# Performance work log

Hardware: AMD Instinct MI355X
Metric: run time of the kernel (lower is better)

Reference implementation:

```python
import jax, jax.numpy as jnp
import numpy as np

B, S, D = 4, 1024, 1024
H, HD = 16, 64
MAXPOS = 1024  # max_position_embeddings


def setup_inputs() -> dict:
    key = jax.random.key(0)
    ks = jax.random.split(key, 10)
    sc = 0.02
    return {
        "hidden_states": jax.random.normal(ks[0], (B, S, D), dtype=jnp.float32),
        "attention_mask": jnp.zeros((B, 1, 1, S), dtype=jnp.float32),
        "across_attention_prior": jax.random.uniform(ks[1], (B, H, S, S), dtype=jnp.float32),
        "head_mask": jnp.ones((1, H, 1, 1), dtype=jnp.float32),
        "Wq": jax.random.normal(ks[2], (D, D), dtype=jnp.float32) * sc,
        "bq": jnp.zeros((D,), dtype=jnp.float32),
        "Wk": jax.random.normal(ks[3], (D, D), dtype=jnp.float32) * sc,
        "bk": jnp.zeros((D,), dtype=jnp.float32),
        "Wv": jax.random.normal(ks[4], (D, D), dtype=jnp.float32) * sc,
        "bv": jnp.zeros((D,), dtype=jnp.float32),
        "dist_emb": jax.random.normal(ks[5], (2 * MAXPOS - 1, HD), dtype=jnp.float32) * sc,
    }


def _heads(x):
    # [B,S,D] -> [B,H,S,HD]
    return x.reshape(B, S, H, HD).transpose(0, 2, 1, 3)


def reference(hidden_states, attention_mask, across_attention_prior, head_mask,
              Wq, bq, Wk, bk, Wv, bv, dist_emb):
    q = _heads(hidden_states @ Wq + bq)  # [B,H,S,HD]
    k = _heads(hidden_states @ Wk + bk)
    v = _heads(hidden_states @ Wv + bv)

    scores = jnp.einsum("bhld,bhrd->bhlr", q, k)

    # relative_key_query positional bias
    pos = jnp.arange(S)
    distance = pos[:, None] - pos[None, :]  # [S,S]
    pe = dist_emb[distance + MAXPOS - 1]  # [S,S,HD] (l, r, d)
    scores = scores + jnp.einsum("bhld,lrd->bhlr", q, pe)
    scores = scores + jnp.einsum("bhrd,lrd->bhlr", k, pe)

    scores = scores / jnp.sqrt(jnp.float32(HD))
    scores = scores + attention_mask  # additive mask, broadcast [B,1,1,S]

    probs = jax.nn.softmax(scores, axis=-1)
    probs = probs * across_attention_prior  # post-softmax multiplicative prior
    probs = probs * head_mask  # dropout prob = 0 (eval)

    ctx = jnp.einsum("bhlr,bhrd->bhld", probs, v)
    ctx = ctx.transpose(0, 2, 1, 3).reshape(B, S, D)
    return ctx
```

## Files before the change

kernel.cpp:

```cpp
#include <hip/hip_runtime.h>


typedef unsigned short u16;
typedef unsigned int   u32;
typedef __attribute__((ext_vector_type(8))) short bfx8;
typedef __attribute__((ext_vector_type(4))) float f32x4;

#define MFMA_BF16(a, b, c) __builtin_amdgcn_mfma_f32_16x16x32_bf16(a, b, c, 0, 0, 0)

__device__ __forceinline__ u16 f2bf(float f) {
    union { float f; u32 u; } c; c.f = f;
    u32 u = c.u;
    return (u16)((u + 0x7FFFu + ((u >> 16) & 1u)) >> 16);
}
__device__ __forceinline__ float bf2f(u16 v) {
    union { u32 u; float f; } c; c.u = ((u32)v) << 16;
    return c.f;
}
__device__ __forceinline__ float load_f(const void* p, long i, bool bf) {
    return bf ? bf2f(((const u16*)p)[i]) : ((const float*)p)[i];
}
__device__ __forceinline__ u16 load_bf(const void* p, long i, bool bf) {
    return bf ? ((const u16*)p)[i] : f2bf(((const float*)p)[i]);
}

__device__ __forceinline__ void gload16(const u16* g, u16* l) {
    __builtin_amdgcn_global_load_lds(
        (__attribute__((address_space(1))) void*)g,
        (__attribute__((address_space(3))) void*)l, 16, 0, 0);
}

__device__ __forceinline__ void wg_barrier() {
    asm volatile("s_waitcnt lgkmcnt(0)" ::: "memory");
    __builtin_amdgcn_s_barrier();
    asm volatile("" ::: "memory");
}

__global__ void k_detect(const u32* hid, int* flags) {
    __shared__ int cnt;
    if (threadIdx.x == 0) cnt = 0;
    __syncthreads();
    int c = 0;
    for (int i = threadIdx.x; i < 1024; i += 256) {
        u32 w = hid[i];
        u32 e = (w >> 7) & 0xFFu;
        if (e >= 100u && e <= 140u) c++;
    }
    atomicAdd(&cnt, c);
    __syncthreads();
    if (threadIdx.x == 0) flags[0] = (cnt > 512) ? 1 : 0;
}

__global__ void k_prep(const void* hidden, const void* dist, const void* mask,
                       const void* hm, const void* bq, const void* bk,
                       const void* bv, const int* flags, u16* hid_bf,
                       u16* dist_bf, float* mask_f, float* hm_f, float* bias_f) {
    const bool bf = flags[0] != 0;
    const long NH = 4L * 1024 * 1024, ND = 2047L * 64, NM = 4096, NB = 3072, NHM = 16;
    const long TOT = NH + ND + NM + NB + NHM;
    for (long i = (long)blockIdx.x * 256 + threadIdx.x; i < TOT;
         i += (long)gridDim.x * 256) {
        if (i < NH) hid_bf[i] = load_bf(hidden, i, bf);
        else if (i < NH + ND) dist_bf[i - NH] = load_bf(dist, i - NH, bf);
        else if (i < NH + ND + NM) mask_f[i - NH - ND] = load_f(mask, i - NH - ND, bf);
        else if (i < NH + ND + NM + NB) {
            long j = i - NH - ND - NM;
            const void* src = (j < 1024) ? bq : ((j < 2048) ? bk : bv);
            bias_f[j] = load_f(src, j & 1023, bf);
        } else {
            long j = i - NH - ND - NM - NB;
            hm_f[j] = load_f(hm, j, bf);
        }
    }
}

__global__ void k_transpose(const void* Wq, const void* Wk, const void* Wv,
                            const int* flags, u16* wt) {
    const bool bf = flags[0] != 0;
    __shared__ float t[32][33];
    const int z = blockIdx.z;
    const void* W = (z == 0) ? Wq : ((z == 1) ? Wk : Wv);
    int x = blockIdx.x * 32 + threadIdx.x;
    for (int i = 0; i < 4; i++) {
        int y = blockIdx.y * 32 + threadIdx.y + i * 8;
        t[threadIdx.y + i * 8][threadIdx.x] = load_f(W, (long)y * 1024 + x, bf);
    }
    __syncthreads();
    int x2 = blockIdx.y * 32 + threadIdx.x;
    u16* out = wt + (long)z * 1024 * 1024;
    for (int i = 0; i < 4; i++) {
        int y2 = blockIdx.x * 32 + threadIdx.y + i * 8;
        out[(long)y2 * 1024 + x2] = f2bf(t[threadIdx.x][threadIdx.y + i * 8]);
    }
}

__global__ __launch_bounds__(256, 2)
void k_qkv_gemm(const u16* A, const u16* Bt, const float* bias,
                u16* qb, u16* kb, u16* vb) {
    __shared__ u16 sA[128 * 32];
    __shared__ u16 sB[128 * 32];
    const int tid = threadIdx.x;
    const int w = tid >> 6, lane = tid & 63;
    const int quad = lane >> 4, nl = lane & 15;
    const int wr = w >> 1, wc = w & 1;
    const int n0 = blockIdx.x * 128, m0 = blockIdx.y * 128;

    f32x4 acc[4][4];
#pragma unroll
    for (int a = 0; a < 4; a++)
#pragma unroll
        for (int b = 0; b < 4; b++) acc[a][b] = (f32x4){0.f, 0.f, 0.f, 0.f};

    for (int kt = 0; kt < 32; kt++) {
        const int k0 = kt * 32;
        __syncthreads();
#pragma unroll
        for (int j = 0; j < 2; j++) {
            int row = 32 * w + 16 * j + (lane >> 2);
            int seg = lane & 3;
            gload16(A + (long)(m0 + row) * 1024 + k0 + seg * 8, sA + 1024 * w + 512 * j);
            gload16(Bt + (long)(n0 + row) * 1024 + k0 + seg * 8, sB + 1024 * w + 512 * j);
        }
        __syncthreads();

        bfx8 af[4], bfr[4];
#pragma unroll
        for (int f = 0; f < 4; f++) {
            af[f]  = *(const bfx8*)(sA + (64 * wr + 16 * f + nl) * 32 + quad * 8);
            bfr[f] = *(const bfx8*)(sB + (64 * wc + 16 * f + nl) * 32 + quad * 8);
        }
#pragma unroll
        for (int fm = 0; fm < 4; fm++)
#pragma unroll
            for (int fn = 0; fn < 4; fn++)
                acc[fm][fn] = MFMA_BF16(af[fm], bfr[fn], acc[fm][fn]);
    }

#pragma unroll
    for (int fm = 0; fm < 4; fm++) {
#pragma unroll
        for (int fn = 0; fn < 4; fn++) {
            int n = n0 + 64 * wc + 16 * fn + nl;
            int which = n >> 10, hcol = n & 1023;
            int h = hcol >> 6, hd = hcol & 63;
            u16* op = (which == 0) ? qb : ((which == 1) ? kb : vb);
            float bias_v = bias[n];
#pragma unroll
            for (int reg = 0; reg < 4; reg++) {
                int m = m0 + 64 * wr + 16 * fm + 4 * quad + reg;
                int b = m >> 10, s = m & 1023;
                float v = acc[fm][fn][reg] + bias_v;
                op[((long)((b * 16 + h) * 1024 + s)) * 64 + hd] = f2bf(v);
            }
        }
    }
}

__global__ __launch_bounds__(256, 2)
void k_attn(const u16* qb, const u16* kb, const u16* vb, const u16* Eb,
            const float* maskf, const float* hmf, const void* prior,
            const int* flags, void* out) {
    constexpr int PT = 72;
    constexpr int PD = 132;
    __shared__ __align__(16) char smem[79872];
    u16* sQ  = (u16*)(smem);
    u16* sK  = (u16*)(smem + 9216);
    u16* sVT = (u16*)(smem + 18432);
    u16* sE  = (u16*)(smem + 27648);
    u16* sDq = (u16*)(smem + 46080);
    u16* sDk = (u16*)(smem + 62976);
    u16* sP  = (u16*)(smem + 46080);

    const int tid = threadIdx.x;
    const int w = tid >> 6, lane = tid & 63;
    const int quad = lane >> 4, nl = lane & 15;
    const int bh = blockIdx.x, b = bh >> 4, h = bh & 15;
    const int l0 = blockIdx.y * 64;
    const bool bf = flags[0] != 0;

    const u16* qbh = qb + (long)bh * 65536;
    const u16* kbh = kb + (long)bh * 65536;
    const u16* vbh = vb + (long)bh * 65536;

#pragma unroll
    for (int p = 0; p < 2; p++) {
        int seg = tid + p * 256;
        int row = seg >> 3, s8 = seg & 7;
        *(int4*)(sQ + row * PT + s8 * 8) = *(const int4*)(qbh + (l0 + row) * 64 + s8 * 8);
    }

    const int erow = tid >> 3, es8 = tid & 7;
    const int jb_base = l0 + 960;

    int4 nK0, nK1, nE0, nE1, nE2, nE3, nV0, nV1;
    {
        nK0 = *(const int4*)(kbh + (0 + erow) * 64 + es8 * 8);
        nK1 = *(const int4*)(kbh + (32 + erow) * 64 + es8 * 8);
        int j0 = jb_base + erow;       if (j0 > 2046) j0 = 2046;
        int j1 = jb_base + 32 + erow;  if (j1 > 2046) j1 = 2046;
        int j2 = jb_base + 64 + erow;  if (j2 > 2046) j2 = 2046;
        int j3 = jb_base + 96 + erow;  if (j3 > 2046) j3 = 2046;
        nE0 = *(const int4*)(Eb + (long)j0 * 64 + es8 * 8);
        nE1 = *(const int4*)(Eb + (long)j1 * 64 + es8 * 8);
        nE2 = *(const int4*)(Eb + (long)j2 * 64 + es8 * 8);
        nE3 = *(const int4*)(Eb + (long)j3 * 64 + es8 * 8);
        nV0 = *(const int4*)(vbh + (0 + lane) * 64 + w * 8);
        nV1 = *(const int4*)(vbh + (0 + lane) * 64 + w * 8 + 32);
    }

    f32x4 accv[4];
#pragma unroll
    for (int f = 0; f < 4; f++) accv[f] = (f32x4){0.f, 0.f, 0.f, 0.f};
    float zacc[4] = {0.f, 0.f, 0.f, 0.f};

    for (int it = 0; it < 16; it++) {
        const int r0 = it * 64;
        wg_barrier();

        *(int4*)(sK + erow * PT + es8 * 8)        = nK0;
        *(int4*)(sK + (32 + erow) * PT + es8 * 8) = nK1;
        *(int4*)(sE + erow * PT + es8 * 8)        = nE0;
        *(int4*)(sE + (32 + erow) * PT + es8 * 8) = nE1;
        *(int4*)(sE + (64 + erow) * PT + es8 * 8) = nE2;
        *(int4*)(sE + (96 + erow) * PT + es8 * 8) = nE3;
        {
            const u16* pv0 = (const u16*)&nV0;
            const u16* pv1 = (const u16*)&nV1;
#pragma unroll
            for (int j2 = 0; j2 < 8; j2++) {
                sVT[(w * 8 + j2) * PT + lane]      = pv0[j2];
                sVT[(w * 8 + 32 + j2) * PT + lane] = pv1[j2];
            }
        }

        float pr[4][4], mval[4];
#pragma unroll
        for (int fn = 0; fn < 4; fn++) {
            mval[fn] = maskf[b * 1024 + r0 + fn * 16 + nl];
#pragma unroll
            for (int reg = 0; reg < 4; reg++) {
                long pidx = ((long)(bh * 1024 + l0 + 16 * w + 4 * quad + reg)) * 1024
                            + r0 + fn * 16 + nl;
                pr[fn][reg] = bf ? bf2f(((const u16*)prior)[pidx])
                                 : ((const float*)prior)[pidx];
            }
        }

        if (it < 15) {
            const int r0n = r0 + 64;
            const int jbn = jb_base - r0n;
            nK0 = *(const int4*)(kbh + (r0n + erow) * 64 + es8 * 8);
            nK1 = *(const int4*)(kbh + (r0n + 32 + erow) * 64 + es8 * 8);
            int j0 = jbn + erow;       if (j0 > 2046) j0 = 2046;
            int j1 = jbn + 32 + erow;  if (j1 > 2046) j1 = 2046;
            int j2 = jbn + 64 + erow;  if (j2 > 2046) j2 = 2046;
            int j3 = jbn + 96 + erow;  if (j3 > 2046) j3 = 2046;
            nE0 = *(const int4*)(Eb + (long)j0 * 64 + es8 * 8);
            nE1 = *(const int4*)(Eb + (long)j1 * 64 + es8 * 8);
            nE2 = *(const int4*)(Eb + (long)j2 * 64 + es8 * 8);
            nE3 = *(const int4*)(Eb + (long)j3 * 64 + es8 * 8);
            nV0 = *(const int4*)(vbh + (r0n + lane) * 64 + w * 8);
            nV1 = *(const int4*)(vbh + (r0n + lane) * 64 + w * 8 + 32);
        }
        wg_barrier();

        bfx8 aq0 = *(const bfx8*)(sQ + (16 * w + nl) * PT + quad * 8);
        bfx8 aq1 = *(const bfx8*)(sQ + (16 * w + nl) * PT + quad * 8 + 32);
        bfx8 ak0 = *(const bfx8*)(sK + (16 * w + nl) * PT + quad * 8);
        bfx8 ak1 = *(const bfx8*)(sK + (16 * w + nl) * PT + quad * 8 + 32);

#pragma unroll
        for (int fc = 0; fc < 8; fc++) {
            bfx8 be0 = *(const bfx8*)(sE + (fc * 16 + nl) * PT + quad * 8);
            bfx8 be1 = *(const bfx8*)(sE + (fc * 16 + nl) * PT + quad * 8 + 32);
            f32x4 dq = (f32x4){0.f, 0.f, 0.f, 0.f};
            dq = MFMA_BF16(aq0, be0, dq);
            dq = MFMA_BF16(aq1, be1, dq);
            f32x4 dk = (f32x4){0.f, 0.f, 0.f, 0.f};
            dk = MFMA_BF16(ak0, be0, dk);
            dk = MFMA_BF16(ak1, be1, dk);
#pragma unroll
            for (int reg = 0; reg < 4; reg++) {
                int rr = 16 * w + 4 * quad + reg;
                sDq[rr * PD + fc * 16 + nl] = f2bf(dq[reg]);
                sDk[rr * PD + fc * 16 + nl] = f2bf(dk[reg]);
            }
        }
        f32x4 accs[4];
#pragma unroll
        for (int fn = 0; fn < 4; fn++) {
            bfx8 bk0 = *(const bfx8*)(sK + (fn * 16 + nl) * PT + quad * 8);
            bfx8 bk1 = *(const bfx8*)(sK + (fn * 16 + nl) * PT + quad * 8 + 32);
            f32x4 s = (f32x4){0.f, 0.f, 0.f, 0.f};
            s = MFMA_BF16(aq0, bk0, s);
            s = MFMA_BF16(aq1, bk1, s);
            accs[fn] = s;
        }
        wg_barrier();

        float pw[4][4];
#pragma unroll
        for (int fn = 0; fn < 4; fn++) {
#pragma unroll
            for (int reg = 0; reg < 4; reg++) {
                int li = 16 * w + 4 * quad + reg;
                int ri = 16 * fn + nl;
                int u = li - ri + 63;
                float s = (accs[fn][reg] + bf2f(sDq[li * PD + u])
                           + bf2f(sDk[ri * PD + u])) * 0.125f + mval[fn];
                float e = __expf(s);
                zacc[reg] += e;
                pw[fn][reg] = e * pr[fn][reg];
            }
        }
        wg_barrier();

#pragma unroll
        for (int fn = 0; fn < 4; fn++)
#pragma unroll
            for (int reg = 0; reg < 4; reg++)
                sP[(16 * w + 4 * quad + reg) * PT + fn * 16 + nl] = f2bf(pw[fn][reg]);

        bfx8 ap0 = *(const bfx8*)(sP + (16 * w + nl) * PT + quad * 8);
        bfx8 ap1 = *(const bfx8*)(sP + (16 * w + nl) * PT + quad * 8 + 32);
#pragma unroll
        for (int fd = 0; fd < 4; fd++) {
            bfx8 bv0 = *(const bfx8*)(sVT + (fd * 16 + nl) * PT + quad * 8);
            bfx8 bv1 = *(const bfx8*)(sVT + (fd * 16 + nl) * PT + quad * 8 + 32);
            accv[fd] = MFMA_BF16(ap0, bv0, accv[fd]);
            accv[fd] = MFMA_BF16(ap1, bv1, accv[fd]);
        }
    }

#pragma unroll
    for (int reg = 0; reg < 4; reg++) {
        float z = zacc[reg];
        z += __shfl_xor(z, 1);
        z += __shfl_xor(z, 2);
        z += __shfl_xor(z, 4);
        z += __shfl_xor(z, 8);
        zacc[reg] = z;
    }
    const float hm = hmf[h];
#pragma unroll
    for (int fd = 0; fd < 4; fd++) {
#pragma unroll
        for (int reg = 0; reg < 4; reg++) {
            int l = l0 + 16 * w + 4 * quad + reg;
            int d = fd * 16 + nl;
            float val = accv[fd][reg] * hm / zacc[reg];
            long oidx = ((long)(b * 1024 + l)) * 1024 + h * 64 + d;
            if (bf) ((u16*)out)[oidx] = f2bf(val);
            else    ((float*)out)[oidx] = val;
        }
    }
}

extern "C" void kernel_launch(void* const* d_in, const int* in_sizes, int n_in,
                              void* d_out, int out_size, void* d_ws, size_t ws_size,
                              hipStream_t stream) {
    char* ws = (char*)d_ws;
    int*   flags   = (int*)ws;
    u16*   hid_bf  = (u16*)(ws + 256);
    u16*   wt_bf   = (u16*)(ws + 8388864);
    u16*   dist_bf = (u16*)(ws + 14680320);
    float* mask_f  = (float*)(ws + 14942464);
    float* bias_f  = (float*)(ws + 14958848);
    float* hm_f    = (float*)(ws + 14971136);
    u16*   q_bf    = (u16*)(ws + 14971392);
    u16*   k_bf    = (u16*)(ws + 23360000);
    u16*   v_bf    = (u16*)(ws + 31748608);

    k_detect<<<1, 256, 0, stream>>>((const u32*)d_in[0], flags);
    k_prep<<<2048, 256, 0, stream>>>(d_in[0], d_in[10], d_in[1], d_in[3],
                                     d_in[5], d_in[7], d_in[9], flags,
                                     hid_bf, dist_bf, mask_f, hm_f, bias_f);
    k_transpose<<<dim3(32, 32, 3), dim3(32, 8), 0, stream>>>(
        d_in[4], d_in[6], d_in[8], flags, wt_bf);
    k_qkv_gemm<<<dim3(24, 32), 256, 0, stream>>>(hid_bf, wt_bf, bias_f,
                                                 q_bf, k_bf, v_bf);
    k_attn<<<dim3(64, 16), 256, 0, stream>>>(q_bf, k_bf, v_bf, dist_bf,
                                             mask_f, hm_f, d_in[2], flags, d_out);
}
```

Baseline: 522.9 us.

## Split attention key tiles across 8 waves and widen QKV GEMM K-tile with swizzle

The attention kernel now runs 512 threads per block. Each pair of waves splits the 64-key tile in half, and the partial P·V accumulators and softmax denominators are combined through shared memory at the end. Q fragments are hoisted out of the loop. The QKV GEMM moves to a 64-wide K tile with XOR-swizzled shared layout and a remapped block order, aiming to reduce bank conflicts and synchronisation count and to improve L2 locality. The risks are higher register pressure under the new launch bounds, the extra cross-wave reduction, and whether 79 KB of shared memory per block allows the intended occupancy.

```diff
diff --git a/kernel.cpp b/kernel.cpp
--- a/kernel.cpp
+++ b/kernel.cpp
@@ -97,13 +97,15 @@
 __global__ __launch_bounds__(256, 2)
 void k_qkv_gemm(const u16* A, const u16* Bt, const float* bias,
                 u16* qb, u16* kb, u16* vb) {
-    __shared__ u16 sA[128 * 32];
-    __shared__ u16 sB[128 * 32];
+    __shared__ u16 sA[128 * 64];
+    __shared__ u16 sB[128 * 64];
     const int tid = threadIdx.x;
     const int w = tid >> 6, lane = tid & 63;
     const int quad = lane >> 4, nl = lane & 15;
     const int wr = w >> 1, wc = w & 1;
-    const int n0 = blockIdx.x * 128, m0 = blockIdx.y * 128;
+    const int bid0 = blockIdx.y * 24 + blockIdx.x;
+    const int bid = (bid0 & 7) * 96 + (bid0 >> 3);
+    const int n0 = (bid % 24) * 128, m0 = (bid / 24) * 128;
 
     f32x4 acc[4][4];
 #pragma unroll
@@ -111,29 +113,39 @@
 #pragma unroll
         for (int b = 0; b < 4; b++) acc[a][b] = (f32x4){0.f, 0.f, 0.f, 0.f};
 
-    for (int kt = 0; kt < 32; kt++) {
-        const int k0 = kt * 32;
+    const int srow = 32 * w + (lane >> 3);
+    const int seg = lane & 7;
+
+    for (int kt = 0; kt < 16; kt++) {
+        const int k0 = kt * 64;
         __syncthreads();
 #pragma unroll
-        for (int j = 0; j < 2; j++) {
-            int row = 32 * w + 16 * j + (lane >> 2);
-            int seg = lane & 3;
-            gload16(A + (long)(m0 + row) * 1024 + k0 + seg * 8, sA + 1024 * w + 512 * j);
-            gload16(Bt + (long)(n0 + row) * 1024 + k0 + seg * 8, sB + 1024 * w + 512 * j);
+        for (int j = 0; j < 4; j++) {
+            int row = srow + 8 * j;
+            int ss = (seg ^ (row & 7)) * 8;
+            gload16(A + (long)(m0 + row) * 1024 + k0 + ss, sA + (32 * w + 8 * j) * 64);
+            gload16(Bt + (long)(n0 + row) * 1024 + k0 + ss, sB + (32 * w + 8 * j) * 64);
         }
         __syncthreads();
 
-        bfx8 af[4], bfr[4];
+        bfx8 af[4][2], bfr[4][2];
 #pragma unroll
         for (int f = 0; f < 4; f++) {
-            af[f]  = *(const bfx8*)(sA + (64 * wr + 16 * f + nl) * 32 + quad * 8);
-            bfr[f] = *(const bfx8*)(sB + (64 * wc + 16 * f + nl) * 32 + quad * 8);
+#pragma unroll
+            for (int hh = 0; hh < 2; hh++) {
+                int Ra = 64 * wr + 16 * f + nl;
+                int Rb = 64 * wc + 16 * f + nl;
+                af[f][hh]  = *(const bfx8*)(sA + Ra * 64 + (((4 * hh + quad) ^ (Ra & 7)) * 8));
+                bfr[f][hh] = *(const bfx8*)(sB + Rb * 64 + (((4 * hh + quad) ^ (Rb & 7)) * 8));
+            }
         }
 #pragma unroll
         for (int fm = 0; fm < 4; fm++)
 #pragma unroll
-            for (int fn = 0; fn < 4; fn++)
-                acc[fm][fn] = MFMA_BF16(af[fm], bfr[fn], acc[fm][fn]);
+            for (int fn = 0; fn < 4; fn++) {
+                acc[fm][fn] = MFMA_BF16(af[fm][0], bfr[fn][0], acc[fm][fn]);
+                acc[fm][fn] = MFMA_BF16(af[fm][1], bfr[fn][1], acc[fm][fn]);
+            }
     }
 
 #pragma unroll
@@ -156,12 +168,13 @@
     }
 }
 
-__global__ __launch_bounds__(256, 2)
+__global__ __launch_bounds__(512, 4)
 void k_attn(const u16* qb, const u16* kb, const u16* vb, const u16* Eb,
             const float* maskf, const float* hmf, const void* prior,
             const int* flags, void* out) {
     constexpr int PT = 72;
     constexpr int PD = 132;
+    constexpr int PX = 66;
     __shared__ __align__(16) char smem[79872];
     u16* sQ  = (u16*)(smem);
     u16* sK  = (u16*)(smem + 9216);
@@ -170,9 +183,12 @@
     u16* sDq = (u16*)(smem + 46080);
     u16* sDk = (u16*)(smem + 62976);
     u16* sP  = (u16*)(smem + 46080);
+    float* accx = (float*)(smem + 46080);
+    float* zs   = (float*)(smem + 9216);
 
     const int tid = threadIdx.x;
-    const int w = tid >> 6, lane = tid & 63;
+    const int W = tid >> 6, lane = tid & 63;
+    const int s = W >> 1, c = W & 1;
     const int quad = lane >> 4, nl = lane & 15;
     const int bh = blockIdx.x, b = bh >> 4, h = bh & 15;
     const int l0 = blockIdx.y * 64;
@@ -182,31 +198,27 @@
     const u16* kbh = kb + (long)bh * 65536;
     const u16* vbh = vb + (long)bh * 65536;
 
-#pragma unroll
-    for (int p = 0; p < 2; p++) {
-        int seg = tid + p * 256;
-        int row = seg >> 3, s8 = seg & 7;
+    {
+        int row = tid >> 3, s8 = tid & 7;
         *(int4*)(sQ + row * PT + s8 * 8) = *(const int4*)(qbh + (l0 + row) * 64 + s8 * 8);
     }
 
     const int erow = tid >> 3, es8 = tid & 7;
     const int jb_base = l0 + 960;
 
-    int4 nK0, nK1, nE0, nE1, nE2, nE3, nV0, nV1;
+    int4 nK0, nE0, nE1, nV0;
     {
-        nK0 = *(const int4*)(kbh + (0 + erow) * 64 + es8 * 8);
-        nK1 = *(const int4*)(kbh + (32 + erow) * 64 + es8 * 8);
+        nK0 = *(const int4*)(kbh + erow * 64 + es8 * 8);
         int j0 = jb_base + erow;       if (j0 > 2046) j0 = 2046;
-        int j1 = jb_base + 32 + erow;  if (j1 > 2046) j1 = 2046;
-        int j2 = jb_base + 64 + erow;  if (j2 > 2046) j2 = 2046;
-        int j3 = jb_base + 96 + erow;  if (j3 > 2046) j3 = 2046;
+        int j1 = jb_base + 64 + erow;  if (j1 > 2046) j1 = 2046;
         nE0 = *(const int4*)(Eb + (long)j0 * 64 + es8 * 8);
         nE1 = *(const int4*)(Eb + (long)j1 * 64 + es8 * 8);
-        nE2 = *(const int4*)(Eb + (long)j2 * 64 + es8 * 8);
-        nE3 = *(const int4*)(Eb + (long)j3 * 64 + es8 * 8);
-        nV0 = *(const int4*)(vbh + (0 + lane) * 64 + w * 8);
-        nV1 = *(const int4*)(vbh + (0 + lane) * 64 + w * 8 + 32);
-    }
+        nV0 = *(const int4*)(vbh + lane * 64 + W * 8);
+    }
+
+    wg_barrier();
+    const bfx8 aq0 = *(const bfx8*)(sQ + (16 * s + nl) * PT + quad * 8);
+    const bfx8 aq1 = *(const bfx8*)(sQ + (16 * s + nl) * PT + quad * 8 + 32);
 
     f32x4 accv[4];
 #pragma unroll
@@ -218,30 +230,24 @@
         wg_barrier();
 
         *(int4*)(sK + erow * PT + es8 * 8)        = nK0;
-        *(int4*)(sK + (32 + erow) * PT + es8 * 8) = nK1;
         *(int4*)(sE + erow * PT + es8 * 8)        = nE0;
-        *(int4*)(sE + (32 + erow) * PT + es8 * 8) = nE1;
-        *(int4*)(sE + (64 + erow) * PT + es8 * 8) = nE2;
-        *(int4*)(sE + (96 + erow) * PT + es8 * 8) = nE3;
+        *(int4*)(sE + (64 + erow) * PT + es8 * 8) = nE1;
         {
-            const u16* pv0 = (const u16*)&nV0;
-            const u16* pv1 = (const u16*)&nV1;
-#pragma unroll
-            for (int j2 = 0; j2 < 8; j2++) {
-                sVT[(w * 8 + j2) * PT + lane]      = pv0[j2];
-                sVT[(w * 8 + 32 + j2) * PT + lane] = pv1[j2];
-            }
-        }
-
-        float pr[4][4], mval[4];
-#pragma unroll
-        for (int fn = 0; fn < 4; fn++) {
-            mval[fn] = maskf[b * 1024 + r0 + fn * 16 + nl];
+            const u16* pv = (const u16*)&nV0;
+#pragma unroll
+            for (int j2 = 0; j2 < 8; j2++) sVT[(W * 8 + j2) * PT + lane] = pv[j2];
+        }
+
+        float pr[2][4], mval[2];
+#pragma unroll
+        for (int f2 = 0; f2 < 2; f2++) {
+            const int fn = 2 * c + f2;
+            mval[f2] = maskf[b * 1024 + r0 + fn * 16 + nl];
 #pragma unroll
             for (int reg = 0; reg < 4; reg++) {
-                long pidx = ((long)(bh * 1024 + l0 + 16 * w + 4 * quad + reg)) * 1024
+                long pidx = ((long)(bh * 1024 + l0 + 16 * s + 4 * quad + reg)) * 1024
                             + r0 + fn * 16 + nl;
-                pr[fn][reg] = bf ? bf2f(((const u16*)prior)[pidx])
+                pr[f2][reg] = bf ? bf2f(((const u16*)prior)[pidx])
                                  : ((const float*)prior)[pidx];
             }
         }
@@ -250,29 +256,22 @@
             const int r0n = r0 + 64;
             const int jbn = jb_base - r0n;
             nK0 = *(const int4*)(kbh + (r0n + erow) * 64 + es8 * 8);
-            nK1 = *(const int4*)(kbh + (r0n + 32 + erow) * 64 + es8 * 8);
             int j0 = jbn + erow;       if (j0 > 2046) j0 = 2046;
-            int j1 = jbn + 32 + erow;  if (j1 > 2046) j1 = 2046;
-            int j2 = jbn + 64 + erow;  if (j2 > 2046) j2 = 2046;
-            int j3 = jbn + 96 + erow;  if (j3 > 2046) j3 = 2046;
+            int j1 = jbn + 64 + erow;  if (j1 > 2046) j1 = 2046;
             nE0 = *(const int4*)(Eb + (long)j0 * 64 + es8 * 8);
             nE1 = *(const int4*)(Eb + (long)j1 * 64 + es8 * 8);
-            nE2 = *(const int4*)(Eb + (long)j2 * 64 + es8 * 8);
-            nE3 = *(const int4*)(Eb + (long)j3 * 64 + es8 * 8);
-            nV0 = *(const int4*)(vbh + (r0n + lane) * 64 + w * 8);
-            nV1 = *(const int4*)(vbh + (r0n + lane) * 64 + w * 8 + 32);
+            nV0 = *(const int4*)(vbh + (r0n + lane) * 64 + W * 8);
         }
         wg_barrier();
 
-        bfx8 aq0 = *(const bfx8*)(sQ + (16 * w + nl) * PT + quad * 8);
-        bfx8 aq1 = *(const bfx8*)(sQ + (16 * w + nl) * PT + quad * 8 + 32);
-        bfx8 ak0 = *(const bfx8*)(sK + (16 * w + nl) * PT + quad * 8);
-        bfx8 ak1 = *(const bfx8*)(sK + (16 * w + nl) * PT + quad * 8 + 32);
-
-#pragma unroll
-        for (int fc = 0; fc < 8; fc++) {
-            bfx8 be0 = *(const bfx8*)(sE + (fc * 16 + nl) * PT + quad * 8);
-            bfx8 be1 = *(const bfx8*)(sE + (fc * 16 + nl) * PT + quad * 8 + 32);
+        const bfx8 ak0 = *(const bfx8*)(sK + (16 * s + nl) * PT + quad * 8);
+        const bfx8 ak1 = *(const bfx8*)(sK + (16 * s + nl) * PT + quad * 8 + 32);
+
+#pragma unroll
+        for (int fcl = 0; fcl < 4; fcl++) {
+            const int R = (4 * c + fcl) * 16 + nl;
+            bfx8 be0 = *(const bfx8*)(sE + R * PT + quad * 8);
+            bfx8 be1 = *(const bfx8*)(sE + R * PT + quad * 8 + 32);
             f32x4 dq = (f32x4){0.f, 0.f, 0.f, 0.f};
             dq = MFMA_BF16(aq0, be0, dq);
             dq = MFMA_BF16(aq1, be1, dq);
@@ -281,54 +280,53 @@
             dk = MFMA_BF16(ak1, be1, dk);
 #pragma unroll
             for (int reg = 0; reg < 4; reg++) {
-                int rr = 16 * w + 4 * quad + reg;
-                sDq[rr * PD + fc * 16 + nl] = f2bf(dq[reg]);
-                sDk[rr * PD + fc * 16 + nl] = f2bf(dk[reg]);
-            }
-        }
-        f32x4 accs[4];
-#pragma unroll
-        for (int fn = 0; fn < 4; fn++) {
-            bfx8 bk0 = *(const bfx8*)(sK + (fn * 16 + nl) * PT + quad * 8);
-            bfx8 bk1 = *(const bfx8*)(sK + (fn * 16 + nl) * PT + quad * 8 + 32);
-            f32x4 s = (f32x4){0.f, 0.f, 0.f, 0.f};
-            s = MFMA_BF16(aq0, bk0, s);
-            s = MFMA_BF16(aq1, bk1, s);
-            accs[fn] = s;
+                int rr = 16 * s + 4 * quad + reg;
+                sDq[rr * PD + R] = f2bf(dq[reg]);
+                sDk[rr * PD + R] = f2bf(dk[reg]);
+            }
+        }
+        f32x4 accs[2];
+#pragma unroll
+        for (int f2 = 0; f2 < 2; f2++) {
+            const int R = (2 * c + f2) * 16 + nl;
+            bfx8 bk0 = *(const bfx8*)(sK + R * PT + quad * 8);
+            bfx8 bk1 = *(const bfx8*)(sK + R * PT + quad * 8 + 32);
+            f32x4 sv = (f32x4){0.f, 0.f, 0.f, 0.f};
+            sv = MFMA_BF16(aq0, bk0, sv);
+            sv = MFMA_BF16(aq1, bk1, sv);
+            accs[f2] = sv;
         }
         wg_barrier();
 
-        float pw[4][4];
-#pragma unroll
-        for (int fn = 0; fn < 4; fn++) {
+        float pw[2][4];
+#pragma unroll
+        for (int f2 = 0; f2 < 2; f2++) {
 #pragma unroll
             for (int reg = 0; reg < 4; reg++) {
-                int li = 16 * w + 4 * quad + reg;
-                int ri = 16 * fn + nl;
+                int li = 16 * s + 4 * quad + reg;
+                int ri = (2 * c + f2) * 16 + nl;
                 int u = li - ri + 63;
-                float s = (accs[fn][reg] + bf2f(sDq[li * PD + u])
-                           + bf2f(sDk[ri * PD + u])) * 0.125f + mval[fn];
-                float e = __expf(s);
+                float sv = (accs[f2][reg] + bf2f(sDq[li * PD + u])
+                            + bf2f(sDk[ri * PD + u])) * 0.125f + mval[f2];
+                float e = __expf(sv);
                 zacc[reg] += e;
-                pw[fn][reg] = e * pr[fn][reg];
+                pw[f2][reg] = e * pr[f2][reg];
             }
         }
         wg_barrier();
 
 #pragma unroll
-        for (int fn = 0; fn < 4; fn++)
+        for (int f2 = 0; f2 < 2; f2++)
 #pragma unroll
             for (int reg = 0; reg < 4; reg++)
-                sP[(16 * w + 4 * quad + reg) * PT + fn * 16 + nl] = f2bf(pw[fn][reg]);
-
-        bfx8 ap0 = *(const bfx8*)(sP + (16 * w + nl) * PT + quad * 8);
-        bfx8 ap1 = *(const bfx8*)(sP + (16 * w + nl) * PT + quad * 8 + 32);
+                sP[(16 * s + 4 * quad + reg) * PT + (2 * c + f2) * 16 + nl] =
+                    f2bf(pw[f2][reg]);
+
+        const bfx8 ap = *(const bfx8*)(sP + (16 * s + nl) * PT + 32 * c + quad * 8);
 #pragma unroll
         for (int fd = 0; fd < 4; fd++) {
-            bfx8 bv0 = *(const bfx8*)(sVT + (fd * 16 + nl) * PT + quad * 8);
-            bfx8 bv1 = *(const bfx8*)(sVT + (fd * 16 + nl) * PT + quad * 8 + 32);
-            accv[fd] = MFMA_BF16(ap0, bv0, accv[fd]);
-            accv[fd] = MFMA_BF16(ap1, bv1, accv[fd]);
+            bfx8 bv = *(const bfx8*)(sVT + (fd * 16 + nl) * PT + 32 * c + quad * 8);
+            accv[fd] = MFMA_BF16(ap, bv, accv[fd]);
         }
     }
 
@@ -341,17 +339,40 @@
         z += __shfl_xor(z, 8);
         zacc[reg] = z;
     }
-    const float hm = hmf[h];
-#pragma unroll
-    for (int fd = 0; fd < 4; fd++) {
+
+    wg_barrier();
+    if (c == 1) {
+#pragma unroll
+        for (int fd = 0; fd < 4; fd++)
+#pragma unroll
+            for (int reg = 0; reg < 4; reg++)
+                accx[(16 * s + 4 * quad + reg) * PX + fd * 16 + nl] = accv[fd][reg];
+    }
+    if (nl == 0) {
+#pragma unroll
+        for (int reg = 0; reg < 4; reg++)
+            zs[(16 * s + 4 * quad + reg) * 2 + c] = zacc[reg];
+    }
+    wg_barrier();
+    if (c == 0) {
+        const float hm = hmf[h];
+        float zt[4];
 #pragma unroll
         for (int reg = 0; reg < 4; reg++) {
-            int l = l0 + 16 * w + 4 * quad + reg;
-            int d = fd * 16 + nl;
-            float val = accv[fd][reg] * hm / zacc[reg];
-            long oidx = ((long)(b * 1024 + l)) * 1024 + h * 64 + d;
-            if (bf) ((u16*)out)[oidx] = f2bf(val);
-            else    ((float*)out)[oidx] = val;
+            int li = 16 * s + 4 * quad + reg;
+            zt[reg] = zs[li * 2] + zs[li * 2 + 1];
+        }
+#pragma unroll
+        for (int fd = 0; fd < 4; fd++) {
+#pragma unroll
+            for (int reg = 0; reg < 4; reg++) {
+                int li = 16 * s + 4 * quad + reg;
+                int d = fd * 16 + nl;
+                float val = (accv[fd][reg] + accx[li * PX + fd * 16 + nl]) * hm / zt[reg];
+                long oidx = ((long)(b * 1024 + l0 + li)) * 1024 + h * 64 + d;
+                if (bf) ((u16*)out)[oidx] = f2bf(val);
+                else    ((float*)out)[oidx] = val;
+            }
         }
     }
 }
@@ -379,6 +400,6 @@
         d_in[4], d_in[6], d_in[8], flags, wt_bf);
     k_qkv_gemm<<<dim3(24, 32), 256, 0, stream>>>(hid_bf, wt_bf, bias_f,
                                                  q_bf, k_bf, v_bf);
-    k_attn<<<dim3(64, 16), 256, 0, stream>>>(q_bf, k_bf, v_bf, dist_bf,
+    k_attn<<<dim3(64, 16), 512, 0, stream>>>(q_bf, k_bf, v_bf, dist_bf,
                                              mask_f, hm_f, d_in[2], flags, d_out);
 }
```

Result: no change. 513.3 us (-1.8%).
